# Optimization experiments

Hardware: AMD Instinct MI355X
Metric: run time of the kernel (lower is better)

The kernel has to match this reference:

```python
import jax, jax.numpy as jnp
import numpy as np

IN_F = 256
OUT_F = 256
HYPER = 128
BATCH = 4096


def setup_inputs() -> dict:
    key = jax.random.key(0)
    ks = jax.random.split(key, 9)
    s_in = 1.0 / np.sqrt(IN_F)
    s_h = 1.0 / np.sqrt(HYPER)
    x = jax.random.normal(ks[0], (BATCH, IN_F), dtype=jnp.float32)
    # weight_gen: Linear(in, hyper) -> ReLU -> Linear(hyper, in*out)
    W1g = jax.random.uniform(ks[1], (IN_F, HYPER), jnp.float32, -s_in, s_in)
    b1g = jax.random.uniform(ks[2], (HYPER,), jnp.float32, -s_in, s_in)
    W2g = jax.random.uniform(ks[3], (HYPER, IN_F * OUT_F), jnp.float32, -s_h, s_h)
    b2g = jax.random.uniform(ks[4], (IN_F * OUT_F,), jnp.float32, -s_h, s_h)
    # bias_gen: Linear(in, hyper) -> ReLU -> Linear(hyper, out)
    W1b = jax.random.uniform(ks[5], (IN_F, HYPER), jnp.float32, -s_in, s_in)
    b1b = jax.random.uniform(ks[6], (HYPER,), jnp.float32, -s_in, s_in)
    W2b = jax.random.uniform(ks[7], (HYPER, OUT_F), jnp.float32, -s_h, s_h)
    b2b = jax.random.uniform(ks[8], (OUT_F,), jnp.float32, -s_h, s_h)
    return {"x": x, "W1g": W1g, "b1g": b1g, "W2g": W2g, "b2g": b2g,
            "W1b": W1b, "b1b": b1b, "W2b": W2b, "b2b": b2b}


def reference(x, W1g, b1g, W2g, b2g, W1b, b1b, W2b, b2b):
    B = x.shape[0]
    # generate per-sample weights [B, out, in]
    hg = jax.nn.relu(x @ W1g + b1g)                      # [B, hyper]
    weights = (hg @ W2g + b2g).reshape(B, OUT_F, IN_F)   # [B, out, in]
    # generate per-sample bias [B, out]
    hb = jax.nn.relu(x @ W1b + b1b)                      # [B, hyper]
    bias = hb @ W2b + b2b                                # [B, out]
    # batched matvec: bmm(weights, x[...,None]) + bias
    out = jnp.einsum('boi,bi->bo', weights, x) + bias    # [B, out]
    return out
```

## Files before the change

### kernel.cpp

```cpp
#include <hip/hip_runtime.h>

#define AS1 __attribute__((address_space(1)))
#define AS3 __attribute__((address_space(3)))

typedef short short8 __attribute__((ext_vector_type(8)));
typedef float f32x16 __attribute__((ext_vector_type(16)));
typedef unsigned short ushort4v __attribute__((ext_vector_type(4)));

#define BATCH 4096
#define IN_F 256
#define OUT_F 256
#define HYP 128
#define HX 129
#define KP (HX * IN_F)

__device__ __forceinline__ float bf2f(unsigned short u) {
  unsigned v = ((unsigned)u) << 16;
  float f;
  __builtin_memcpy(&f, &v, 4);
  return f;
}
__device__ __forceinline__ unsigned short f2bf(float f) {
  unsigned u;
  __builtin_memcpy(&u, &f, 4);
  unsigned r = u + 0x7fffu + ((u >> 16) & 1u);
  return (unsigned short)(r >> 16);
}

__device__ __forceinline__ void gld_lds16(const unsigned short* g, unsigned short* s) {
  __builtin_amdgcn_global_load_lds((const AS1 unsigned int*)g, (AS3 unsigned int*)s, 16, 0, 0);
}

__global__ void k_buildV(const float* __restrict__ W2g, const float* __restrict__ b2g,
                         unsigned short* __restrict__ Vb) {
  const int cid = blockIdx.x * 256 + threadIdx.x;
  const int ic = cid & 31;
  const int pair = cid >> 5;
  const int h = pair % HX;
  const int o = pair / HX;
  const float* src = (h < HYP) ? (W2g + (size_t)h * (OUT_F * IN_F) + o * IN_F + ic * 8)
                               : (b2g + o * IN_F + ic * 8);
  const float4 v0 = ((const float4*)src)[0];
  const float4 v1 = ((const float4*)src)[1];
  uint4 pk;
  pk.x = (unsigned)f2bf(v0.x) | ((unsigned)f2bf(v0.y) << 16);
  pk.y = (unsigned)f2bf(v0.z) | ((unsigned)f2bf(v0.w) << 16);
  pk.z = (unsigned)f2bf(v1.x) | ((unsigned)f2bf(v1.y) << 16);
  pk.w = (unsigned)f2bf(v1.z) | ((unsigned)f2bf(v1.w) << 16);
  *(uint4*)(Vb + (size_t)o * KP + h * IN_F + ic * 8) = pk;
}

__global__ __launch_bounds__(256) void k_pre(const float* __restrict__ x,
                                             const float* __restrict__ W1g, const float* __restrict__ b1g,
                                             const float* __restrict__ W1b, const float* __restrict__ b1b,
                                             const float* __restrict__ W2b, const float* __restrict__ b2b,
                                             unsigned short* __restrict__ hgbT,
                                             unsigned short* __restrict__ xb,
                                             float* __restrict__ out) {
  __shared__ float xl[16 * IN_F];
  __shared__ float hbl[16 * HYP];
  __shared__ unsigned short hgt[HYP * 16];
  const int t = threadIdx.x;
  const int r0 = blockIdx.x * 16;
  for (int j0 = 0; j0 < 16 * IN_F; j0 += 256) {
    const float v = x[(size_t)r0 * IN_F + j0 + t];
    xl[j0 + t] = v;
    xb[(size_t)r0 * IN_F + j0 + t] = f2bf(v);
  }
  __syncthreads();
  const int h = t & 127;
  const int rb = (t >> 7) * 8;
  float ag[8] = {0.f, 0.f, 0.f, 0.f, 0.f, 0.f, 0.f, 0.f};
  float av[8] = {0.f, 0.f, 0.f, 0.f, 0.f, 0.f, 0.f, 0.f};
  for (int i = 0; i < IN_F; ++i) {
    const float wg = W1g[i * HYP + h];
    const float wb = W1b[i * HYP + h];
#pragma unroll
    for (int r = 0; r < 8; ++r) {
      const float xv = xl[(rb + r) * IN_F + i];
      ag[r] += xv * wg;
      av[r] += xv * wb;
    }
  }
  const float bg = b1g[h], bb = b1b[h];
#pragma unroll
  for (int r = 0; r < 8; ++r) {
    float g = ag[r] + bg; g = g > 0.f ? g : 0.f;
    float v = av[r] + bb; v = v > 0.f ? v : 0.f;
    hgt[h * 16 + rb + r] = f2bf(g);
    hbl[(rb + r) * HYP + h] = v;
  }
  __syncthreads();
  {
    const int h2 = t >> 1, part = t & 1;
    const uint4 pk = *(const uint4*)&hgt[h2 * 16 + part * 8];
    *(uint4*)&hgbT[(size_t)h2 * BATCH + r0 + part * 8] = pk;
  }
  float acc[16];
#pragma unroll
  for (int r = 0; r < 16; ++r) acc[r] = 0.f;
  for (int hh = 0; hh < HYP; ++hh) {
    const float w = W2b[hh * OUT_F + t];
#pragma unroll
    for (int r = 0; r < 16; ++r) acc[r] += hbl[r * HYP + hh] * w;
  }
  const float bo = b2b[t];
#pragma unroll
  for (int r = 0; r < 16; ++r) out[(size_t)(r0 + r) * OUT_F + t] = acc[r] + bo;
}

__global__ __launch_bounds__(256, 1) void k_gemm(const unsigned short* __restrict__ Vb,
                                                 const unsigned short* __restrict__ hgbT,
                                                 const unsigned short* __restrict__ xb,
                                                 float* __restrict__ out) {
  __shared__ __align__(16) unsigned short Bl[2][64 * 256];
  __shared__ __align__(16) unsigned short hgs[33 * 256];
  const int tid = threadIdx.x;
  const int lane = tid & 63;
  const int wave = tid >> 6;
  const int l31 = lane & 31;
  const int hi = lane >> 5;
  const int m0 = blockIdx.x * 256;
  const int o0 = blockIdx.y * 64;
  const int z = blockIdx.z;
  const int hBeg = (z * HX) >> 2;
  const int hEnd = ((z + 1) * HX) >> 2;
  const int nh = hEnd - hBeg;

  for (int idx = tid; idx < nh * 256; idx += 256) {
    const int hl = idx >> 8;
    const int hh = hBeg + hl;
    hgs[idx] = (hh == HYP) ? (unsigned short)0x3F80
                           : hgbT[(size_t)hh * BATCH + m0 + (idx & 255)];
  }

  const int mrow0 = m0 + wave * 64 + l31;
  const int mrow1 = mrow0 + 32;
  uint4 xf0[16], xf1[16];
#pragma unroll
  for (int j = 0; j < 16; ++j) {
    xf0[j] = *(const uint4*)(xb + (size_t)mrow0 * IN_F + j * 16 + hi * 8);
    xf1[j] = *(const uint4*)(xb + (size_t)mrow1 * IN_F + j * 16 + hi * 8);
  }

  const int nB = tid >> 5;
  const int p = tid & 31;
  const int cs = p ^ (nB & 7);
  const unsigned short* gsrc = Vb + (size_t)(o0 + nB) * KP + cs * 8 + (size_t)hBeg * IN_F;

  f32x16 zv;
#pragma unroll
  for (int i = 0; i < 16; ++i) zv[i] = 0.0f;
  f32x16 acc00 = zv, acc01 = zv, acc10 = zv, acc11 = zv;
  f32x16 ah00 = zv, ah01 = zv, ah10 = zv, ah11 = zv;

#pragma unroll
  for (int j = 0; j < 8; ++j)
    gld_lds16(gsrc + (size_t)j * 8 * KP, &Bl[0][(tid + 256 * j) * 8]);
  __syncthreads();

  for (int r = 0; r < nh; ++r) {
    const int buf = r & 1;
    if (r + 1 < nh) {
      const unsigned short* gs = gsrc + (size_t)(r + 1) * IN_F;
#pragma unroll
      for (int j = 0; j < 8; ++j)
        gld_lds16(gs + (size_t)j * 8 * KP, &Bl[buf ^ 1][(tid + 256 * j) * 8]);
    }
    float hgf0[16], hgf1[16];
#pragma unroll
    for (int q = 0; q < 4; ++q) {
      const ushort4v v0 = *(const ushort4v*)&hgs[r * 256 + wave * 64 + 4 * hi + q * 8];
      const ushort4v v1 = *(const ushort4v*)&hgs[r * 256 + wave * 64 + 32 + 4 * hi + q * 8];
#pragma unroll
      for (int e = 0; e < 4; ++e) {
        hgf0[q * 4 + e] = bf2f(v0[e]);
        hgf1[q * 4 + e] = bf2f(v1[e]);
      }
    }
    const unsigned short* bp = &Bl[buf][0];
#pragma unroll
    for (int ic = 0; ic < 4; ++ic) {
#pragma unroll
      for (int t = 0; t < 4; ++t) {
        const int c0 = ic * 8 + t * 2 + hi;
        const int pr = c0 ^ (l31 & 7);
        const short8 b0 = *(const short8*)(bp + l31 * 256 + pr * 8);
        const short8 b1 = *(const short8*)(bp + (32 + l31) * 256 + pr * 8);
        const short8 a0 = __builtin_bit_cast(short8, xf0[ic * 4 + t]);
        const short8 a1 = __builtin_bit_cast(short8, xf1[ic * 4 + t]);
        ah00 = __builtin_amdgcn_mfma_f32_32x32x16_bf16(a0, b0, ah00, 0, 0, 0);
        ah01 = __builtin_amdgcn_mfma_f32_32x32x16_bf16(a0, b1, ah01, 0, 0, 0);
        ah10 = __builtin_amdgcn_mfma_f32_32x32x16_bf16(a1, b0, ah10, 0, 0, 0);
        ah11 = __builtin_amdgcn_mfma_f32_32x32x16_bf16(a1, b1, ah11, 0, 0, 0);
      }
    }
#pragma unroll
    for (int g = 0; g < 16; ++g) {
      acc00[g] += hgf0[g] * ah00[g];
      acc01[g] += hgf0[g] * ah01[g];
      acc10[g] += hgf1[g] * ah10[g];
      acc11[g] += hgf1[g] * ah11[g];
    }
    ah00 = zv; ah01 = zv; ah10 = zv; ah11 = zv;
    __syncthreads();
  }

  const int mb = m0 + wave * 64 + 4 * hi;
#pragma unroll
  for (int g = 0; g < 16; ++g) {
    const int row0 = mb + (g & 3) + 8 * (g >> 2);
    atomicAdd(&out[(size_t)row0 * OUT_F + o0 + l31], acc00[g]);
    atomicAdd(&out[(size_t)row0 * OUT_F + o0 + 32 + l31], acc01[g]);
    atomicAdd(&out[(size_t)(row0 + 32) * OUT_F + o0 + l31], acc10[g]);
    atomicAdd(&out[(size_t)(row0 + 32) * OUT_F + o0 + 32 + l31], acc11[g]);
  }
}

extern "C" void kernel_launch(void* const* d_in, const int* in_sizes, int n_in,
                              void* d_out, int out_size, void* d_ws, size_t ws_size,
                              hipStream_t stream) {
  const float* x = (const float*)d_in[0];
  const float* W1g = (const float*)d_in[1];
  const float* b1g = (const float*)d_in[2];
  const float* W2g = (const float*)d_in[3];
  const float* b2g = (const float*)d_in[4];
  const float* W1b = (const float*)d_in[5];
  const float* b1b = (const float*)d_in[6];
  const float* W2b = (const float*)d_in[7];
  const float* b2b = (const float*)d_in[8];
  float* out = (float*)d_out;

  char* ws = (char*)d_ws;
  const size_t szV = (size_t)OUT_F * KP * 2;
  const size_t szHg = (size_t)HYP * BATCH * 2;
  unsigned short* Vb = (unsigned short*)ws;
  unsigned short* hgbT = (unsigned short*)(ws + szV);
  unsigned short* xb = (unsigned short*)(ws + szV + szHg);

  hipLaunchKernelGGL(k_buildV, dim3(OUT_F * HX / 8), dim3(256), 0, stream, W2g, b2g, Vb);
  hipLaunchKernelGGL(k_pre, dim3(BATCH / 16), dim3(256), 0, stream,
                     x, W1g, b1g, W1b, b1b, W2b, b2b, hgbT, xb, out);
  hipLaunchKernelGGL(k_gemm, dim3(BATCH / 256, OUT_F / 64, 4), dim3(256), 0, stream,
                     Vb, hgbT, xb, out);
}
```

Baseline: 219.3 us.

## Fuse weight-build into prep kernel and split gemm tile across 8 waves

Merges the V-matrix bf16 conversion kernel into the prep kernel as extra blocks, which removes one launch and lets both kinds of work run side by side. The gemm kernel moves from 256 to 512 threads, with each wave now covering one 32-column slab instead of two. This halves the accumulator registers per wave and allows two blocks per CU. Blocks are remapped with a 1D grid swizzle so that CUs sharing a group reuse cached V and x data, at the cost of more waves loading the same x fragments and hg values.

```diff
diff --git a/kernel.cpp b/kernel.cpp
--- a/kernel.cpp
+++ b/kernel.cpp
@@ -13,6 +13,7 @@
 #define HYP 128
 #define HX 129
 #define KP (HX * IN_F)
+#define NBUILD (OUT_F * HX / 8)
 
 __device__ __forceinline__ float bf2f(unsigned short u) {
   unsigned v = ((unsigned)u) << 16;
@@ -31,36 +32,40 @@
   __builtin_amdgcn_global_load_lds((const AS1 unsigned int*)g, (AS3 unsigned int*)s, 16, 0, 0);
 }
 
-__global__ void k_buildV(const float* __restrict__ W2g, const float* __restrict__ b2g,
-                         unsigned short* __restrict__ Vb) {
-  const int cid = blockIdx.x * 256 + threadIdx.x;
-  const int ic = cid & 31;
-  const int pair = cid >> 5;
-  const int h = pair % HX;
-  const int o = pair / HX;
-  const float* src = (h < HYP) ? (W2g + (size_t)h * (OUT_F * IN_F) + o * IN_F + ic * 8)
-                               : (b2g + o * IN_F + ic * 8);
-  const float4 v0 = ((const float4*)src)[0];
-  const float4 v1 = ((const float4*)src)[1];
-  uint4 pk;
-  pk.x = (unsigned)f2bf(v0.x) | ((unsigned)f2bf(v0.y) << 16);
-  pk.y = (unsigned)f2bf(v0.z) | ((unsigned)f2bf(v0.w) << 16);
-  pk.z = (unsigned)f2bf(v1.x) | ((unsigned)f2bf(v1.y) << 16);
-  pk.w = (unsigned)f2bf(v1.z) | ((unsigned)f2bf(v1.w) << 16);
-  *(uint4*)(Vb + (size_t)o * KP + h * IN_F + ic * 8) = pk;
-}
-
-__global__ __launch_bounds__(256) void k_pre(const float* __restrict__ x,
-                                             const float* __restrict__ W1g, const float* __restrict__ b1g,
-                                             const float* __restrict__ W1b, const float* __restrict__ b1b,
-                                             const float* __restrict__ W2b, const float* __restrict__ b2b,
-                                             unsigned short* __restrict__ hgbT,
-                                             unsigned short* __restrict__ xb,
-                                             float* __restrict__ out) {
+__global__ __launch_bounds__(256) void k_prep(
+    const float* __restrict__ x,
+    const float* __restrict__ W1g, const float* __restrict__ b1g,
+    const float* __restrict__ W2g, const float* __restrict__ b2g,
+    const float* __restrict__ W1b, const float* __restrict__ b1b,
+    const float* __restrict__ W2b, const float* __restrict__ b2b,
+    unsigned short* __restrict__ Vb,
+    unsigned short* __restrict__ hgbT,
+    unsigned short* __restrict__ xb,
+    float* __restrict__ out) {
   __shared__ float xl[16 * IN_F];
   __shared__ float hbl[16 * HYP];
   __shared__ unsigned short hgt[HYP * 16];
   const int t = threadIdx.x;
+
+  if (blockIdx.x >= 256) {
+    const int cid = (blockIdx.x - 256) * 256 + t;
+    const int ic = cid & 31;
+    const int pair = cid >> 5;
+    const int h = pair % HX;
+    const int o = pair / HX;
+    const float* src = (h < HYP) ? (W2g + (size_t)h * (OUT_F * IN_F) + o * IN_F + ic * 8)
+                                 : (b2g + o * IN_F + ic * 8);
+    const float4 v0 = ((const float4*)src)[0];
+    const float4 v1 = ((const float4*)src)[1];
+    uint4 pk;
+    pk.x = (unsigned)f2bf(v0.x) | ((unsigned)f2bf(v0.y) << 16);
+    pk.y = (unsigned)f2bf(v0.z) | ((unsigned)f2bf(v0.w) << 16);
+    pk.z = (unsigned)f2bf(v1.x) | ((unsigned)f2bf(v1.y) << 16);
+    pk.w = (unsigned)f2bf(v1.z) | ((unsigned)f2bf(v1.w) << 16);
+    *(uint4*)(Vb + (size_t)o * KP + h * IN_F + ic * 8) = pk;
+    return;
+  }
+
   const int r0 = blockIdx.x * 16;
   for (int j0 = 0; j0 < 16 * IN_F; j0 += 256) {
     const float v = x[(size_t)r0 * IN_F + j0 + t];
@@ -109,7 +114,7 @@
   for (int r = 0; r < 16; ++r) out[(size_t)(r0 + r) * OUT_F + t] = acc[r] + bo;
 }
 
-__global__ __launch_bounds__(256, 1) void k_gemm(const unsigned short* __restrict__ Vb,
+__global__ __launch_bounds__(512, 2) void k_gemm(const unsigned short* __restrict__ Vb,
                                                  const unsigned short* __restrict__ hgbT,
                                                  const unsigned short* __restrict__ xb,
                                                  float* __restrict__ out) {
@@ -120,21 +125,32 @@
   const int wave = tid >> 6;
   const int l31 = lane & 31;
   const int hi = lane >> 5;
-  const int m0 = blockIdx.x * 256;
-  const int o0 = blockIdx.y * 64;
-  const int z = blockIdx.z;
+  const int wm = wave & 3;
+  const int wo = wave >> 2;
+
+  const int bid = blockIdx.x;
+  const int c = bid & 7;
+  const int t2 = bid >> 3;
+  const int xm = t2 & 15;
+  const int g8 = t2 >> 4;
+  const int grp = c + 8 * g8;
+  const int yo = grp & 3;
+  const int z = grp >> 2;
+
+  const int m0 = xm * 256;
+  const int o0 = yo * 64;
   const int hBeg = (z * HX) >> 2;
   const int hEnd = ((z + 1) * HX) >> 2;
   const int nh = hEnd - hBeg;
 
-  for (int idx = tid; idx < nh * 256; idx += 256) {
+  for (int idx = tid; idx < nh * 256; idx += 512) {
     const int hl = idx >> 8;
     const int hh = hBeg + hl;
     hgs[idx] = (hh == HYP) ? (unsigned short)0x3F80
                            : hgbT[(size_t)hh * BATCH + m0 + (idx & 255)];
   }
 
-  const int mrow0 = m0 + wave * 64 + l31;
+  const int mrow0 = m0 + wm * 64 + l31;
   const int mrow1 = mrow0 + 32;
   uint4 xf0[16], xf1[16];
 #pragma unroll
@@ -151,12 +167,12 @@
   f32x16 zv;
 #pragma unroll
   for (int i = 0; i < 16; ++i) zv[i] = 0.0f;
-  f32x16 acc00 = zv, acc01 = zv, acc10 = zv, acc11 = zv;
-  f32x16 ah00 = zv, ah01 = zv, ah10 = zv, ah11 = zv;
-
-#pragma unroll
-  for (int j = 0; j < 8; ++j)
-    gld_lds16(gsrc + (size_t)j * 8 * KP, &Bl[0][(tid + 256 * j) * 8]);
+  f32x16 acc0 = zv, acc1 = zv;
+  f32x16 ah0 = zv, ah1 = zv;
+
+#pragma unroll
+  for (int j = 0; j < 4; ++j)
+    gld_lds16(gsrc + (size_t)j * 16 * KP, &Bl[0][(tid + 512 * j) * 8]);
   __syncthreads();
 
   for (int r = 0; r < nh; ++r) {
@@ -164,56 +180,45 @@
     if (r + 1 < nh) {
       const unsigned short* gs = gsrc + (size_t)(r + 1) * IN_F;
 #pragma unroll
-      for (int j = 0; j < 8; ++j)
-        gld_lds16(gs + (size_t)j * 8 * KP, &Bl[buf ^ 1][(tid + 256 * j) * 8]);
-    }
-    float hgf0[16], hgf1[16];
-#pragma unroll
-    for (int q = 0; q < 4; ++q) {
-      const ushort4v v0 = *(const ushort4v*)&hgs[r * 256 + wave * 64 + 4 * hi + q * 8];
-      const ushort4v v1 = *(const ushort4v*)&hgs[r * 256 + wave * 64 + 32 + 4 * hi + q * 8];
-#pragma unroll
-      for (int e = 0; e < 4; ++e) {
-        hgf0[q * 4 + e] = bf2f(v0[e]);
-        hgf1[q * 4 + e] = bf2f(v1[e]);
-      }
+      for (int j = 0; j < 4; ++j)
+        gld_lds16(gs + (size_t)j * 16 * KP, &Bl[buf ^ 1][(tid + 512 * j) * 8]);
     }
     const unsigned short* bp = &Bl[buf][0];
+    const int rowb = wo * 32 + l31;
 #pragma unroll
     for (int ic = 0; ic < 4; ++ic) {
 #pragma unroll
       for (int t = 0; t < 4; ++t) {
         const int c0 = ic * 8 + t * 2 + hi;
         const int pr = c0 ^ (l31 & 7);
-        const short8 b0 = *(const short8*)(bp + l31 * 256 + pr * 8);
-        const short8 b1 = *(const short8*)(bp + (32 + l31) * 256 + pr * 8);
+        const short8 b0 = *(const short8*)(bp + rowb * 256 + pr * 8);
         const short8 a0 = __builtin_bit_cast(short8, xf0[ic * 4 + t]);
         const short8 a1 = __builtin_bit_cast(short8, xf1[ic * 4 + t]);
-        ah00 = __builtin_amdgcn_mfma_f32_32x32x16_bf16(a0, b0, ah00, 0, 0, 0);
-        ah01 = __builtin_amdgcn_mfma_f32_32x32x16_bf16(a0, b1, ah01, 0, 0, 0);
-        ah10 = __builtin_amdgcn_mfma_f32_32x32x16_bf16(a1, b0, ah10, 0, 0, 0);
-        ah11 = __builtin_amdgcn_mfma_f32_32x32x16_bf16(a1, b1, ah11, 0, 0, 0);
+        ah0 = __builtin_amdgcn_mfma_f32_32x32x16_bf16(a0, b0, ah0, 0, 0, 0);
+        ah1 = __builtin_amdgcn_mfma_f32_32x32x16_bf16(a1, b0, ah1, 0, 0, 0);
       }
     }
 #pragma unroll
-    for (int g = 0; g < 16; ++g) {
-      acc00[g] += hgf0[g] * ah00[g];
-      acc01[g] += hgf0[g] * ah01[g];
-      acc10[g] += hgf1[g] * ah10[g];
-      acc11[g] += hgf1[g] * ah11[g];
-    }
-    ah00 = zv; ah01 = zv; ah10 = zv; ah11 = zv;
+    for (int q = 0; q < 4; ++q) {
+      const ushort4v v0 = *(const ushort4v*)&hgs[r * 256 + wm * 64 + 4 * hi + q * 8];
+      const ushort4v v1 = *(const ushort4v*)&hgs[r * 256 + wm * 64 + 32 + 4 * hi + q * 8];
+#pragma unroll
+      for (int e = 0; e < 4; ++e) {
+        acc0[q * 4 + e] += bf2f(v0[e]) * ah0[q * 4 + e];
+        acc1[q * 4 + e] += bf2f(v1[e]) * ah1[q * 4 + e];
+      }
+    }
+    ah0 = zv; ah1 = zv;
     __syncthreads();
   }
 
-  const int mb = m0 + wave * 64 + 4 * hi;
+  const int mb = m0 + wm * 64 + 4 * hi;
+  const int col = o0 + wo * 32 + l31;
 #pragma unroll
   for (int g = 0; g < 16; ++g) {
     const int row0 = mb + (g & 3) + 8 * (g >> 2);
-    atomicAdd(&out[(size_t)row0 * OUT_F + o0 + l31], acc00[g]);
-    atomicAdd(&out[(size_t)row0 * OUT_F + o0 + 32 + l31], acc01[g]);
-    atomicAdd(&out[(size_t)(row0 + 32) * OUT_F + o0 + l31], acc10[g]);
-    atomicAdd(&out[(size_t)(row0 + 32) * OUT_F + o0 + 32 + l31], acc11[g]);
+    atomicAdd(&out[(size_t)row0 * OUT_F + col], acc0[g]);
+    atomicAdd(&out[(size_t)(row0 + 32) * OUT_F + col], acc1[g]);
   }
 }
 
@@ -238,9 +243,8 @@
   unsigned short* hgbT = (unsigned short*)(ws + szV);
   unsigned short* xb = (unsigned short*)(ws + szV + szHg);
 
-  hipLaunchKernelGGL(k_buildV, dim3(OUT_F * HX / 8), dim3(256), 0, stream, W2g, b2g, Vb);
-  hipLaunchKernelGGL(k_pre, dim3(BATCH / 16), dim3(256), 0, stream,
-                     x, W1g, b1g, W1b, b1b, W2b, b2b, hgbT, xb, out);
-  hipLaunchKernelGGL(k_gemm, dim3(BATCH / 256, OUT_F / 64, 4), dim3(256), 0, stream,
+  hipLaunchKernelGGL(k_prep, dim3(256 + NBUILD), dim3(256), 0, stream,
+                     x, W1g, b1g, W2g, b2g, W1b, b1b, W2b, b2b, Vb, hgbT, xb, out);
+  hipLaunchKernelGGL(k_gemm, dim3(256), dim3(512), 0, stream,
                      Vb, hgbT, xb, out);
 }
```

Result: faster. 200.4 us (-8.7%).
